# Kernel tuning notes

Measured on AMD Instinct MI355X. Metric: run time of the kernel, lower is better.

The kernel has to match this reference:

```python
import jax, jax.numpy as jnp
import numpy as np

B, T, D, H, E, O, A = 8192, 223, 7, 128, 50, 29, 9
IMPUTE_W, LABEL_W = 0.3, 1.0

def setup_inputs() -> dict:
    key = jax.random.key(0)
    ks = jax.random.split(key, 32)
    u = lambda k, shape, fan: jax.random.uniform(k, shape, jnp.float32, -1.0/np.sqrt(fan), 1.0/np.sqrt(fan))
    return {
        'values':    jax.random.normal(ks[0], (B, T, D), jnp.float32),
        'masks':     (jax.random.uniform(ks[1], (B, T, D)) < 0.8).astype(jnp.float32),
        'deltas':    jax.random.uniform(ks[2], (B, T, D), jnp.float32) * 5.0,
        'probs':     jax.nn.softmax(jax.random.normal(ks[3], (B, O), jnp.float32), axis=1),
        'ancillary': jax.random.normal(ks[4], (B, A), jnp.float32),
        'labels':    jax.random.randint(ks[5], (B,), 0, O, jnp.int32),
        'W_td_h': u(ks[6], (H, D), H),  'b_td_h': u(ks[7], (H,), H),
        'W_td_x': u(ks[8], (D, D), D),  'b_td_x': u(ks[9], (D,), D),
        'W_hist': u(ks[10], (D, H), H), 'b_hist': u(ks[11], (D,), H),
        'W_feat': u(ks[12], (D, D), D), 'b_feat': u(ks[13], (D,), D),
        'W_comb': u(ks[14], (D, 2*D), 2*D), 'b_comb': u(ks[15], (D,), 2*D),
        'W_ih': u(ks[16], (4*H, 2*D), H), 'W_hh': u(ks[17], (4*H, H), H),
        'b_ih': u(ks[18], (4*H,), H),     'b_hh': u(ks[19], (4*H,), H),
        'W_anc': u(ks[20], (E, A), A),    'b_anc': u(ks[21], (E,), A),
        'W_cat': u(ks[22], (H, H + E), H + E), 'b_cat': u(ks[23], (H,), H + E),
        'W_out': u(ks[24], (O, H), H),    'b_out': u(ks[25], (O,), H),
    }

def _rits_forward(values, masks, deltas, probs, ancillary,
                  W_td_h, b_td_h, W_td_x, b_td_x, W_hist, b_hist,
                  W_feat, b_feat, W_comb, b_comb, W_ih, W_hh, b_ih, b_hh,
                  W_anc, b_anc, W_cat, b_cat, W_out, b_out):
    Bn = values.shape[0]
    td_x_diag = jnp.diag(W_td_x)                     # diag=True decay uses only diagonal
    Wf = W_feat * (1.0 - jnp.eye(D, dtype=W_feat.dtype))

    def step(carry, xt):
        h, c, xl = carry
        x, m, d = xt                                  # each [B, D]
        gamma_h = jnp.exp(-jax.nn.relu(d @ W_td_h.T + b_td_h))   # [B, H]
        gamma_x = jnp.exp(-jax.nn.relu(d * td_x_diag + b_td_x))  # [B, D]
        h = h * gamma_h
        x_h = h @ W_hist.T + b_hist
        msum = jnp.sum(m) + 1e-5
        xl = xl + jnp.sum(jnp.abs(x - x_h) * m) / msum
        x_c = m * x + (1.0 - m) * x_h
        z_h = x_c @ Wf.T + b_feat
        xl = xl + jnp.sum(jnp.abs(x - z_h) * m) / msum
        alpha = jnp.concatenate([gamma_x, m], axis=1) @ W_comb.T + b_comb
        c_h = alpha * z_h + (1.0 - alpha) * x_h
        xl = xl + jnp.sum(jnp.abs(x - c_h) * m) / msum
        c_c = m * x + (1.0 - m) * c_h
        inputs = jnp.concatenate([c_c, m], axis=1)    # [B, 2D]
        gates = inputs @ W_ih.T + b_ih + h @ W_hh.T + b_hh  # [B, 4H]
        i, f, g, o = jnp.split(gates, 4, axis=1)
        c = jax.nn.sigmoid(f) * c + jax.nn.sigmoid(i) * jnp.tanh(g)
        h = jax.nn.sigmoid(o) * jnp.tanh(c)
        return (h, c, xl), c_c

    h0 = jnp.zeros((Bn, H), values.dtype)
    c0 = jnp.zeros((Bn, H), values.dtype)
    xs = (jnp.swapaxes(values, 0, 1), jnp.swapaxes(masks, 0, 1), jnp.swapaxes(deltas, 0, 1))
    (h, c, x_loss), imps = jax.lax.scan(step, (h0, c0, jnp.float32(0.0)), xs)
    imputations = jnp.swapaxes(imps, 0, 1)           # [B, T, D]

    x_loss = x_loss * IMPUTE_W
    anc = jax.nn.relu(ancillary @ W_anc.T + b_anc)
    h = jax.nn.relu(jnp.concatenate([h, anc], axis=1) @ W_cat.T + b_cat)
    y_h = jax.nn.softmax(h @ W_out.T + b_out, axis=1)
    y_loss = jnp.sum((y_h - probs) ** 2) / (Bn + 1e-5) * LABEL_W
    return x_loss, y_loss, x_loss + y_loss, y_h, imputations

def reference(values, masks, deltas, probs, ancillary, labels,
              W_td_h, b_td_h, W_td_x, b_td_x, W_hist, b_hist,
              W_feat, b_feat, W_comb, b_comb, W_ih, W_hh, b_ih, b_hh,
              W_anc, b_anc, W_cat, b_cat, W_out, b_out):
    x_loss, y_loss, loss, y_h, imputations = _rits_forward(
        values, masks, deltas, probs, ancillary,
        W_td_h, b_td_h, W_td_x, b_td_x, W_hist, b_hist,
        W_feat, b_feat, W_comb, b_comb, W_ih, W_hh, b_ih, b_hh,
        W_anc, b_anc, W_cat, b_cat, W_out, b_out)
    return (x_loss, y_loss, loss, y_h, imputations, labels)
```

## Files before the change

kernel.cpp:

```cpp
#include <hip/hip_runtime.h>
#include <math.h>

#define B_ 8192
#define T_ 223
#define D_ 7
#define H_ 128
#define E_ 50
#define O_ 29
#define A_ 9
#define TD_ (T_*D_)
#define NB 32
#define NTHR 512
#define MB 8
#define MS_BG 128

#define WS_MINV  0
#define WS_ACC   (WS_MINV + T_)
#define WS_WCATT (WS_ACC + 2)
#define WS_HFIN  (WS_WCATT + 178*H_)

#define OUT_YH  3
#define OUT_IMP (OUT_YH + B_*O_)
#define OUT_LAB (OUT_IMP + B_*T_*D_)

typedef __attribute__((ext_vector_type(8))) short short8;
typedef __attribute__((ext_vector_type(4))) float floatx4;
#define MFMA16(Av,Bv,Cv) __builtin_amdgcn_mfma_f32_16x16x32_bf16((Av),(Bv),(Cv),0,0,0)

__device__ __forceinline__ unsigned short f2bf(float f) {
    unsigned int u = __builtin_bit_cast(unsigned int, f);
    return (unsigned short)((u + 0x7FFFu + ((u >> 16) & 1u)) >> 16);
}
__device__ __forceinline__ float bf2f(unsigned short s) {
    unsigned int u = ((unsigned int)s) << 16;
    return __builtin_bit_cast(float, u);
}
__device__ __forceinline__ float rcp_(float x)  { return __builtin_amdgcn_rcpf(x); }
__device__ __forceinline__ float sigm(float x)  { return rcp_(1.f + __expf(-x)); }
__device__ __forceinline__ float tanh_(float x) { return 1.f - 2.f*rcp_(1.f + __expf(2.f*x)); }

__global__ void rits_prep(const float* __restrict__ W_cat, float* __restrict__ ws)
{
    int idx = blockIdx.x * 256 + threadIdx.x;
    if (idx < H_*178) {
        int j = idx / 178, k = idx - j*178;
        ws[WS_WCATT + k*H_ + j] = W_cat[idx];
    }
    if (idx < T_) ws[WS_MINV + idx] = 0.f;
    if (idx < 2) ws[WS_ACC + idx] = 0.f;
}

__global__ void rits_msum(const float* __restrict__ masks, float* __restrict__ ws)
{
    const int tc = blockIdx.x % 7;
    const int bg = blockIdx.x / 7;
    const int t0 = tc * 32;
    const int nt = (t0 + 32 <= T_) ? 32 : (T_ - t0);
    const int ncol = nt * D_;
    const int tid = threadIdx.x;
    __shared__ float sums[224];
    float s = 0.f;
    if (tid < ncol) {
        const int bpg = B_ / MS_BG;
        const float* p = masks + (size_t)bg * bpg * TD_ + (size_t)t0 * D_ + tid;
        #pragma unroll 4
        for (int b = 0; b < bpg; ++b) s += p[(size_t)b * TD_];
    }
    if (tid < 224) sums[tid] = (tid < ncol) ? s : 0.f;
    __syncthreads();
    if (tid < 32) {
        float r = 0.f;
        #pragma unroll
        for (int q = 0; q < 7; ++q) r += sums[tid*7 + q];
        if (t0 + tid < T_) atomicAdd(&ws[WS_MINV + t0 + tid], r);
    }
}

__global__ __launch_bounds__(NTHR, 2) void rits_main(
    const float* __restrict__ values, const float* __restrict__ masks, const float* __restrict__ deltas,
    const float* __restrict__ W_td_h, const float* __restrict__ b_td_h,
    const float* __restrict__ W_td_x, const float* __restrict__ b_td_x,
    const float* __restrict__ W_hist, const float* __restrict__ b_hist,
    const float* __restrict__ W_feat, const float* __restrict__ b_feat,
    const float* __restrict__ W_comb, const float* __restrict__ b_comb,
    const float* __restrict__ W_ih, const float* __restrict__ W_hh,
    const float* __restrict__ b_ih, const float* __restrict__ b_hh,
    float* __restrict__ ws, float* __restrict__ out)
{
    __shared__ __attribute__((aligned(16))) unsigned short hbuf[NB*168];
    __shared__ __attribute__((aligned(16))) unsigned short dbuf[NB*72];
    __shared__ __attribute__((aligned(16))) unsigned short whis_lds[16*136];
    __shared__ float xs[NB*8], msh[NB*8], dsl[NB*8];
    __shared__ float xh_l[NB*8], xc_l[NB*8], gx_l[NB*8];
    __shared__ float bhist_l[8], tdx_l[8], btdx_l[8];
    __shared__ float impbuf[NB*16*7];
    __shared__ float red[8];

    const int tid  = threadIdx.x;
    const int b0   = blockIdx.x * NB;
    const int lane = tid & 63;
    const int w    = tid >> 6;
    const int quad = lane >> 4;
    const int l15  = lane & 15;

    for (int i = tid; i < NB*168; i += NTHR) hbuf[i] = 0;
    for (int i = tid; i < NB*72;  i += NTHR) dbuf[i] = 0;
    for (int i = tid; i < 16*136; i += NTHR) {
        int r = i / 136, c = i - r*136;
        whis_lds[i] = (r < 7 && c < 128) ? f2bf(W_hist[r*H_ + c]) : 0;
    }
    if (tid < 8) {
        bhist_l[tid] = (tid < 7) ? b_hist[tid] : 0.f;
        tdx_l[tid]   = (tid < 7) ? W_td_x[tid*D_ + tid] : 0.f;
        btdx_l[tid]  = (tid < 7) ? b_td_x[tid] : 0.f;
    }

    short8 whhf[4][4];
    short8 winf[4];
    short8 wtdf;
    float  biasg_r[4][4];
    float  btdh_r[4];
    {
        union UU { short8 v; unsigned short u[8]; } fr;
        #pragma unroll
        for (int c = 0; c < 4; ++c) {
            const int j = (c*8 + w)*16 + l15;
            #pragma unroll
            for (int s = 0; s < 4; ++s) {
                const float* p = W_hh + j*H_ + s*32 + quad*8;
                #pragma unroll
                for (int e = 0; e < 8; ++e) fr.u[e] = f2bf(p[e]);
                whhf[c][s] = fr.v;
            }
            #pragma unroll
            for (int e = 0; e < 8; ++e) {
                int k = quad*8 + e;
                fr.u[e] = (k < 14) ? f2bf(W_ih[j*14 + k]) : (unsigned short)0;
            }
            winf[c] = fr.v;
            #pragma unroll
            for (int r = 0; r < 4; ++r) {
                int jj = (c*8 + w)*16 + quad*4 + r;
                biasg_r[c][r] = b_ih[jj] + b_hh[jj];
            }
        }
        #pragma unroll
        for (int e = 0; e < 8; ++e) {
            int k = quad*8 + e;
            fr.u[e] = (k < 7) ? f2bf(W_td_h[(w*16 + l15)*D_ + k]) : (unsigned short)0;
        }
        wtdf = fr.v;
        #pragma unroll
        for (int r = 0; r < 4; ++r) btdh_r[r] = b_td_h[w*16 + quad*4 + r];
    }

    const bool ldr = (tid < NB*D_);
    const int  lb  = tid / D_, li = tid - (tid/D_)*D_;
    float wfr[7], wcr[14], bfr = 0.f, bcr = 0.f;
    if (ldr) {
        #pragma unroll
        for (int k = 0; k < 7; ++k)  wfr[k] = (k == li) ? 0.f : W_feat[li*D_ + k];
        #pragma unroll
        for (int k = 0; k < 14; ++k) wcr[k] = W_comb[li*14 + k];
        bfr = b_feat[li];  bcr = b_comb[li];
    }

    float c_st[2][4] = {{0,0,0,0},{0,0,0,0}};
    float lacc = 0.f;

    const long gbase = (long)(b0 + lb)*TD_ + li;
    float rx = 0.f, rm = 0.f, rd = 0.f;
    if (ldr) { rx = values[gbase]; rm = masks[gbase]; rd = deltas[gbase]; }

    const float* msums = ws + WS_MINV;

    for (int t = 0; t < T_; ++t) {
        if (ldr) { xs[lb*8+li] = rx; msh[lb*8+li] = rm; dsl[lb*8+li] = rd; }
        __syncthreads();
        if (ldr) {
            if (t + 1 < T_) {
                const long g = gbase + (long)(t+1)*D_;
                rx = values[g]; rm = masks[g]; rd = deltas[g];
            }
            dbuf[lb*72 + li] = f2bf(rd);
        }

        floatx4 acc[4][2];
        #pragma unroll
        for (int c = 0; c < 4; ++c)
            #pragma unroll
            for (int nt = 0; nt < 2; ++nt) {
                floatx4 a = { biasg_r[c][0], biasg_r[c][1], biasg_r[c][2], biasg_r[c][3] };
                acc[c][nt] = a;
            }
        floatx4 xh0 = {0,0,0,0}, xh1 = {0,0,0,0};
        #pragma unroll
        for (int s = 0; s < 4; ++s) {
            short8 hb0 = *(const short8*)&hbuf[l15*168       + s*32 + quad*8];
            short8 hb1 = *(const short8*)&hbuf[(16+l15)*168  + s*32 + quad*8];
            #pragma unroll
            for (int c = 0; c < 4; ++c) {
                acc[c][0] = MFMA16(whhf[c][s], hb0, acc[c][0]);
                acc[c][1] = MFMA16(whhf[c][s], hb1, acc[c][1]);
            }
            if (w == 7) {
                short8 wh = *(const short8*)&whis_lds[l15*136 + s*32 + quad*8];
                xh0 = MFMA16(wh, hb0, xh0);
                xh1 = MFMA16(wh, hb1, xh1);
            }
        }
        if (w == 7 && quad < 2) {
            #pragma unroll
            for (int nt = 0; nt < 2; ++nt) {
                const int b = nt*16 + l15;
                floatx4 xv = nt ? xh1 : xh0;
                #pragma unroll
                for (int r = 0; r < 4; ++r) {
                    const int i = quad*4 + r;
                    if (i < 7) {
                        float xhv = xv[r] + bhist_l[i];
                        float x = xs[b*8+i], m = msh[b*8+i], d = dsl[b*8+i];
                        xh_l[b*8+i] = xhv;
                        xc_l[b*8+i] = m*x + (1.f-m)*xhv;
                        gx_l[b*8+i] = __expf(-fmaxf(fmaf(d, tdx_l[i], btdx_l[i]), 0.f));
                    }
                }
            }
        }
        __syncthreads();

        floatx4 g0 = {0,0,0,0}, g1 = {0,0,0,0};
        const bool dec = (t + 1 < T_);
        if (dec) {
            short8 df0 = *(const short8*)&dbuf[l15*72      + quad*8];
            short8 df1 = *(const short8*)&dbuf[(16+l15)*72 + quad*8];
            floatx4 z = {0,0,0,0};
            g0 = MFMA16(wtdf, df0, z);
            g1 = MFMA16(wtdf, df1, z);
        }

        if (ldr) {
            const int b = lb, i = li;
            const float invt = rcp_(msums[t] + 1e-5f);
            const float x = xs[b*8+i], m = msh[b*8+i];
            float zh = bfr;
            #pragma unroll
            for (int k = 0; k < 7; ++k) zh = fmaf(wfr[k], xc_l[b*8+k], zh);
            float al = bcr;
            #pragma unroll
            for (int k = 0; k < 7; ++k) al = fmaf(wcr[k],   gx_l[b*8+k], al);
            #pragma unroll
            for (int k = 0; k < 7; ++k) al = fmaf(wcr[7+k], msh[b*8+k], al);
            const float xhv = xh_l[b*8+i];
            const float ch  = al*zh + (1.f-al)*xhv;
            const float cc  = m*x + (1.f-m)*ch;
            impbuf[(b*16 + (t & 15))*7 + i] = cc;
            hbuf[b*168 + 128 + i] = f2bf(cc);
            hbuf[b*168 + 135 + i] = f2bf(m);
            lacc = fmaf((fabsf(x-xhv) + fabsf(x-zh) + fabsf(x-ch)) * m, invt, lacc);
        }
        __syncthreads();

        {
            short8 ib0 = *(const short8*)&hbuf[l15*168      + 128 + quad*8];
            short8 ib1 = *(const short8*)&hbuf[(16+l15)*168 + 128 + quad*8];
            #pragma unroll
            for (int c = 0; c < 4; ++c) {
                acc[c][0] = MFMA16(winf[c], ib0, acc[c][0]);
                acc[c][1] = MFMA16(winf[c], ib1, acc[c][1]);
            }
        }
        #pragma unroll
        for (int nt = 0; nt < 2; ++nt) {
            const int b = nt*16 + l15;
            floatx4 gg = nt ? g1 : g0;
            float hnv[4];
            #pragma unroll
            for (int r = 0; r < 4; ++r) {
                float ig = acc[0][nt][r], fg = acc[1][nt][r];
                float gv = acc[2][nt][r], og = acc[3][nt][r];
                float cn = sigm(fg)*c_st[nt][r] + sigm(ig)*tanh_(gv);
                c_st[nt][r] = cn;
                float hn = sigm(og)*tanh_(cn);
                if (dec) hn *= __expf(-fmaxf(gg[r] + btdh_r[r], 0.f));
                hnv[r] = hn;
            }
            uint2 pk;
            pk.x = (unsigned)f2bf(hnv[0]) | ((unsigned)f2bf(hnv[1]) << 16);
            pk.y = (unsigned)f2bf(hnv[2]) | ((unsigned)f2bf(hnv[3]) << 16);
            *(uint2*)&hbuf[b*168 + w*16 + quad*4] = pk;
        }

        if ((t & 15) == 15 || t == T_ - 1) {
            const int t0 = t & ~15;
            const int b  = tid >> 4, c16 = tid & 15;
            if (t0 + c16 <= t) {
                float* gp = out + (size_t)OUT_IMP + (size_t)(b0+b)*TD_ + (size_t)(t0+c16)*D_;
                const float* lp = &impbuf[(b*16 + c16)*7];
                #pragma unroll
                for (int e = 0; e < 7; ++e) gp[e] = lp[e];
            }
        }
    }
    __syncthreads();

    for (int off = 32; off > 0; off >>= 1) lacc += __shfl_down(lacc, off, 64);
    if ((tid & 63) == 0) red[tid >> 6] = lacc;
    __syncthreads();
    if (tid == 0) {
        float s = 0.f;
        #pragma unroll
        for (int q = 0; q < 8; ++q) s += red[q];
        atomicAdd(&ws[WS_ACC], s);
    }
    for (int i = tid; i < NB*H_; i += NTHR) {
        int b = i >> 7, j = i & 127;
        ws[WS_HFIN + (size_t)(b0+b)*H_ + j] = bf2f(hbuf[b*168 + j]);
    }
}

__global__ __launch_bounds__(128) void rits_head(
    const float* __restrict__ probs, const float* __restrict__ ancillary, const int* __restrict__ labels,
    const float* __restrict__ W_anc, const float* __restrict__ b_anc,
    const float* __restrict__ b_cat,
    const float* __restrict__ W_out, const float* __restrict__ b_out,
    float* __restrict__ ws, float* __restrict__ out)
{
    __shared__ float hb[MB*H_];
    __shared__ float ancl[MB*52];
    __shared__ float hc[MB*H_];
    __shared__ float lg[MB*32];
    __shared__ float smx[MB], sinv[MB], ysum[MB];
    __shared__ float sq[MB*32];
    const int tid = threadIdx.x;
    const int bb0 = blockIdx.x * MB;

    for (int i = tid; i < MB*H_; i += 128) hb[i] = ws[WS_HFIN + (size_t)bb0*H_ + i];
    for (int i = tid; i < MB*E_; i += 128) {
        int b = i / E_, e = i - b*E_;
        float s = b_anc[e];
        #pragma unroll
        for (int a = 0; a < A_; ++a) s = fmaf(ancillary[(bb0+b)*A_ + a], W_anc[e*A_ + a], s);
        ancl[b*52+e] = fmaxf(s, 0.f);
    }
    __syncthreads();
    {
        const int j = tid;
        float s[MB];
        #pragma unroll
        for (int b = 0; b < MB; ++b) s[b] = b_cat[j];
        const float* wc = ws + WS_WCATT;
        for (int k = 0; k < H_; ++k) {
            float wv = wc[k*H_ + j];
            #pragma unroll
            for (int b = 0; b < MB; ++b) s[b] = fmaf(hb[b*H_+k], wv, s[b]);
        }
        for (int k = 0; k < E_; ++k) {
            float wv = wc[(H_+k)*H_ + j];
            #pragma unroll
            for (int b = 0; b < MB; ++b) s[b] = fmaf(ancl[b*52+k], wv, s[b]);
        }
        #pragma unroll
        for (int b = 0; b < MB; ++b) hc[b*H_+j] = fmaxf(s[b], 0.f);
    }
    __syncthreads();
    for (int i = tid; i < MB*O_; i += 128) {
        int b = i / O_, o = i - b*O_;
        float s = b_out[o];
        for (int k = 0; k < H_; ++k) s = fmaf(hc[b*H_+k], W_out[o*H_+k], s);
        lg[b*32+o] = s;
    }
    __syncthreads();
    if (tid < MB) {
        float mx = -1e30f;
        for (int o = 0; o < O_; ++o) mx = fmaxf(mx, lg[tid*32+o]);
        float se = 0.f;
        for (int o = 0; o < O_; ++o) se += __expf(lg[tid*32+o] - mx);
        smx[tid] = mx; sinv[tid] = 1.f / se;
    }
    __syncthreads();
    for (int i = tid; i < MB*O_; i += 128) {
        int b = i / O_, o = i - b*O_;
        float y = __expf(lg[b*32+o] - smx[b]) * sinv[b];
        out[OUT_YH + (size_t)(bb0+b)*O_ + o] = y;
        float d = y - probs[(size_t)(bb0+b)*O_ + o];
        sq[b*32+o] = d*d;
    }
    __syncthreads();
    if (tid < MB) {
        float s = 0.f;
        for (int o = 0; o < O_; ++o) s += sq[tid*32+o];
        ysum[tid] = s;
        out[OUT_LAB + bb0 + tid] = (float)labels[bb0 + tid];
    }
    __syncthreads();
    if (tid == 0) {
        float s = 0.f;
        #pragma unroll
        for (int b = 0; b < MB; ++b) s += ysum[b];
        atomicAdd(&ws[WS_ACC+1], s);
    }
}

__global__ void rits_fin(const float* __restrict__ ws, float* __restrict__ out)
{
    if (blockIdx.x == 0 && threadIdx.x == 0) {
        float xl = ws[WS_ACC] * 0.3f;
        float yl = ws[WS_ACC+1] * (1.0f / (8192.0f + 1e-5f));
        out[0] = xl; out[1] = yl; out[2] = xl + yl;
    }
}

extern "C" void kernel_launch(void* const* d_in, const int* in_sizes, int n_in,
                              void* d_out, int out_size, void* d_ws, size_t ws_size,
                              hipStream_t stream)
{
    const float* values = (const float*)d_in[0];
    const float* masks  = (const float*)d_in[1];
    const float* deltas = (const float*)d_in[2];
    const float* probs  = (const float*)d_in[3];
    const float* ancil  = (const float*)d_in[4];
    const int*   labels = (const int*)  d_in[5];
    const float* W_td_h = (const float*)d_in[6];
    const float* b_td_h = (const float*)d_in[7];
    const float* W_td_x = (const float*)d_in[8];
    const float* b_td_x = (const float*)d_in[9];
    const float* W_hist = (const float*)d_in[10];
    const float* b_hist = (const float*)d_in[11];
    const float* W_feat = (const float*)d_in[12];
    const float* b_feat = (const float*)d_in[13];
    const float* W_comb = (const float*)d_in[14];
    const float* b_comb = (const float*)d_in[15];
    const float* W_ih   = (const float*)d_in[16];
    const float* W_hh   = (const float*)d_in[17];
    const float* b_ih   = (const float*)d_in[18];
    const float* b_hh   = (const float*)d_in[19];
    const float* W_anc  = (const float*)d_in[20];
    const float* b_anc  = (const float*)d_in[21];
    const float* W_cat  = (const float*)d_in[22];
    const float* b_cat  = (const float*)d_in[23];
    const float* W_out  = (const float*)d_in[24];
    const float* b_out  = (const float*)d_in[25];
    float* ws  = (float*)d_ws;
    float* out = (float*)d_out;

    hipLaunchKernelGGL(rits_prep, dim3((H_*178 + 255)/256), dim3(256), 0, stream, W_cat, ws);
    hipLaunchKernelGGL(rits_msum, dim3(7*MS_BG), dim3(256), 0, stream, masks, ws);
    hipLaunchKernelGGL(rits_main, dim3(B_/NB), dim3(NTHR), 0, stream,
                       values, masks, deltas, W_td_h, b_td_h, W_td_x, b_td_x,
                       W_hist, b_hist, W_feat, b_feat, W_comb, b_comb,
                       W_ih, W_hh, b_ih, b_hh, ws, out);
    hipLaunchKernelGGL(rits_head, dim3(B_/MB), dim3(128), 0, stream,
                       probs, ancil, labels, W_anc, b_anc, b_cat, W_out, b_out, ws, out);
    hipLaunchKernelGGL(rits_fin, dim3(1), dim3(1), 0, stream, ws, out);
}
```

Measured before the change: 933.8 us.

## Fold gate biases and mask input into MFMA, redistribute decay and xc compute

Folds the LSTM gate bias and the mask half of the input projection into one MFMA that runs earlier, using a buffer that holds mask, delta and a constant-one column. The temporal-decay bias moves into the decay MFMA the same way. The x_c and gamma_x work moves from the single wave-7 serial section to the per-element loader threads. Biases are now rounded to bf16 inside the MFMA, which costs some precision, and the critical section between barriers gets shorter.

```diff
diff --git a/kernel.cpp b/kernel.cpp
--- a/kernel.cpp
+++ b/kernel.cpp
@@ -88,11 +88,11 @@
     float* __restrict__ ws, float* __restrict__ out)
 {
     __shared__ __attribute__((aligned(16))) unsigned short hbuf[NB*168];
-    __shared__ __attribute__((aligned(16))) unsigned short dbuf[NB*72];
+    __shared__ __attribute__((aligned(16))) unsigned short bbuf[NB*32];
     __shared__ __attribute__((aligned(16))) unsigned short whis_lds[16*136];
-    __shared__ float xs[NB*8], msh[NB*8], dsl[NB*8];
-    __shared__ float xh_l[NB*8], xc_l[NB*8], gx_l[NB*8];
-    __shared__ float bhist_l[8], tdx_l[8], btdx_l[8];
+    __shared__ float xm_l[NB*18];
+    __shared__ float gx_l[NB*9];
+    __shared__ float xh_l[NB*10];
     __shared__ float impbuf[NB*16*7];
     __shared__ float red[8];
 
@@ -104,22 +104,22 @@
     const int l15  = lane & 15;
 
     for (int i = tid; i < NB*168; i += NTHR) hbuf[i] = 0;
-    for (int i = tid; i < NB*72;  i += NTHR) dbuf[i] = 0;
+    for (int i = tid; i < NB*32;  i += NTHR) bbuf[i] = 0;
     for (int i = tid; i < 16*136; i += NTHR) {
         int r = i / 136, c = i - r*136;
         whis_lds[i] = (r < 7 && c < 128) ? f2bf(W_hist[r*H_ + c]) : 0;
     }
-    if (tid < 8) {
-        bhist_l[tid] = (tid < 7) ? b_hist[tid] : 0.f;
-        tdx_l[tid]   = (tid < 7) ? W_td_x[tid*D_ + tid] : 0.f;
-        btdx_l[tid]  = (tid < 7) ? b_td_x[tid] : 0.f;
+    __syncthreads();
+    if (tid < NB) {
+        bbuf[tid*32 + 7]  = 0x3F80;
+        bbuf[tid*32 + 15] = 0x3F80;
     }
 
     short8 whhf[4][4];
-    short8 winf[4];
+    short8 winf_c[4];
+    short8 winf_mb[4];
     short8 wtdf;
-    float  biasg_r[4][4];
-    float  btdh_r[4];
+    float  bh_r[4];
     {
         union UU { short8 v; unsigned short u[8]; } fr;
         #pragma unroll
@@ -135,34 +135,44 @@
             #pragma unroll
             for (int e = 0; e < 8; ++e) {
                 int k = quad*8 + e;
-                fr.u[e] = (k < 14) ? f2bf(W_ih[j*14 + k]) : (unsigned short)0;
-            }
-            winf[c] = fr.v;
-            #pragma unroll
-            for (int r = 0; r < 4; ++r) {
-                int jj = (c*8 + w)*16 + quad*4 + r;
-                biasg_r[c][r] = b_ih[jj] + b_hh[jj];
-            }
-        }
+                fr.u[e] = (k < 7) ? f2bf(W_ih[j*14 + k]) : (unsigned short)0;
+            }
+            winf_c[c] = fr.v;
+            #pragma unroll
+            for (int e = 0; e < 8; ++e) {
+                int k = quad*8 + e;
+                float v = (k < 7) ? W_ih[j*14 + 7 + k]
+                        : ((k == 7) ? (b_ih[j] + b_hh[j]) : 0.f);
+                fr.u[e] = f2bf(v);
+            }
+            winf_mb[c] = fr.v;
+        }
+        const int j2 = w*16 + l15;
         #pragma unroll
         for (int e = 0; e < 8; ++e) {
             int k = quad*8 + e;
-            fr.u[e] = (k < 7) ? f2bf(W_td_h[(w*16 + l15)*D_ + k]) : (unsigned short)0;
+            float v = (k >= 8 && k < 15) ? W_td_h[j2*D_ + (k - 8)]
+                    : ((k == 15) ? b_td_h[j2] : 0.f);
+            fr.u[e] = f2bf(v);
         }
         wtdf = fr.v;
         #pragma unroll
-        for (int r = 0; r < 4; ++r) btdh_r[r] = b_td_h[w*16 + quad*4 + r];
+        for (int r = 0; r < 4; ++r) {
+            int f = quad*4 + r;
+            bh_r[r] = (quad < 2 && f < 7) ? b_hist[f] : 0.f;
+        }
     }
 
     const bool ldr = (tid < NB*D_);
     const int  lb  = tid / D_, li = tid - (tid/D_)*D_;
-    float wfr[7], wcr[14], bfr = 0.f, bcr = 0.f;
+    float wfr[7], wcr[14], bfr = 0.f, bcr = 0.f, tdx_own = 0.f, btdx_own = 0.f;
     if (ldr) {
         #pragma unroll
         for (int k = 0; k < 7; ++k)  wfr[k] = (k == li) ? 0.f : W_feat[li*D_ + k];
         #pragma unroll
         for (int k = 0; k < 14; ++k) wcr[k] = W_comb[li*14 + k];
         bfr = b_feat[li];  bcr = b_comb[li];
+        tdx_own = W_td_x[li*D_ + li];  btdx_own = b_td_x[li];
     }
 
     float c_st[2][4] = {{0,0,0,0},{0,0,0,0}};
@@ -175,24 +185,24 @@
     const float* msums = ws + WS_MINV;
 
     for (int t = 0; t < T_; ++t) {
-        if (ldr) { xs[lb*8+li] = rx; msh[lb*8+li] = rm; dsl[lb*8+li] = rd; }
+        if (ldr) {
+            float2 s2 = { rx, rm };
+            *(float2*)&xm_l[lb*18 + 2*li] = s2;
+            gx_l[lb*9 + li] = __expf(-fmaxf(fmaf(rd, tdx_own, btdx_own), 0.f));
+            bbuf[lb*32 + li] = f2bf(rm);
+        }
         __syncthreads();
-        if (ldr) {
-            if (t + 1 < T_) {
-                const long g = gbase + (long)(t+1)*D_;
-                rx = values[g]; rm = masks[g]; rd = deltas[g];
-            }
-            dbuf[lb*72 + li] = f2bf(rd);
+        if (ldr && t + 1 < T_) {
+            const long g = gbase + (long)(t+1)*D_;
+            rx = values[g]; rm = masks[g]; rd = deltas[g];
+            bbuf[lb*32 + 8 + li] = f2bf(rd);
         }
 
         floatx4 acc[4][2];
         #pragma unroll
         for (int c = 0; c < 4; ++c)
             #pragma unroll
-            for (int nt = 0; nt < 2; ++nt) {
-                floatx4 a = { biasg_r[c][0], biasg_r[c][1], biasg_r[c][2], biasg_r[c][3] };
-                acc[c][nt] = a;
-            }
+            for (int nt = 0; nt < 2; ++nt) { floatx4 z = {0,0,0,0}; acc[c][nt] = z; }
         floatx4 xh0 = {0,0,0,0}, xh1 = {0,0,0,0};
         #pragma unroll
         for (int s = 0; s < 4; ++s) {
@@ -214,49 +224,51 @@
             for (int nt = 0; nt < 2; ++nt) {
                 const int b = nt*16 + l15;
                 floatx4 xv = nt ? xh1 : xh0;
-                #pragma unroll
-                for (int r = 0; r < 4; ++r) {
-                    const int i = quad*4 + r;
-                    if (i < 7) {
-                        float xhv = xv[r] + bhist_l[i];
-                        float x = xs[b*8+i], m = msh[b*8+i], d = dsl[b*8+i];
-                        xh_l[b*8+i] = xhv;
-                        xc_l[b*8+i] = m*x + (1.f-m)*xhv;
-                        gx_l[b*8+i] = __expf(-fmaxf(fmaf(d, tdx_l[i], btdx_l[i]), 0.f));
-                    }
-                }
+                float2 p0 = { xv[0] + bh_r[0], xv[1] + bh_r[1] };
+                float2 p1 = { xv[2] + bh_r[2], xv[3] + bh_r[3] };
+                *(float2*)&xh_l[b*10 + quad*4]     = p0;
+                *(float2*)&xh_l[b*10 + quad*4 + 2] = p1;
             }
         }
         __syncthreads();
 
+        const bool dec = (t + 1 < T_);
         floatx4 g0 = {0,0,0,0}, g1 = {0,0,0,0};
-        const bool dec = (t + 1 < T_);
-        if (dec) {
-            short8 df0 = *(const short8*)&dbuf[l15*72      + quad*8];
-            short8 df1 = *(const short8*)&dbuf[(16+l15)*72 + quad*8];
-            floatx4 z = {0,0,0,0};
-            g0 = MFMA16(wtdf, df0, z);
-            g1 = MFMA16(wtdf, df1, z);
+        {
+            short8 bb0 = *(const short8*)&bbuf[l15*32      + quad*8];
+            short8 bb1 = *(const short8*)&bbuf[(16+l15)*32 + quad*8];
+            #pragma unroll
+            for (int c = 0; c < 4; ++c) {
+                acc[c][0] = MFMA16(winf_mb[c], bb0, acc[c][0]);
+                acc[c][1] = MFMA16(winf_mb[c], bb1, acc[c][1]);
+            }
+            if (dec) {
+                floatx4 z = {0,0,0,0};
+                g0 = MFMA16(wtdf, bb0, z);
+                g1 = MFMA16(wtdf, bb1, z);
+            }
         }
 
         if (ldr) {
             const int b = lb, i = li;
             const float invt = rcp_(msums[t] + 1e-5f);
-            const float x = xs[b*8+i], m = msh[b*8+i];
-            float zh = bfr;
-            #pragma unroll
-            for (int k = 0; k < 7; ++k) zh = fmaf(wfr[k], xc_l[b*8+k], zh);
-            float al = bcr;
-            #pragma unroll
-            for (int k = 0; k < 7; ++k) al = fmaf(wcr[k],   gx_l[b*8+k], al);
-            #pragma unroll
-            for (int k = 0; k < 7; ++k) al = fmaf(wcr[7+k], msh[b*8+k], al);
-            const float xhv = xh_l[b*8+i];
-            const float ch  = al*zh + (1.f-al)*xhv;
-            const float cc  = m*x + (1.f-m)*ch;
+            const float x = xm_l[b*18 + 2*i], m = xm_l[b*18 + 2*i + 1];
+            const float xhv = xh_l[b*10 + i];
+            float zh = bfr, al = bcr;
+            #pragma unroll
+            for (int k = 0; k < 7; ++k) {
+                const float xk  = xm_l[b*18 + 2*k];
+                const float mk  = xm_l[b*18 + 2*k + 1];
+                const float xhk = xh_l[b*10 + k];
+                const float xck = mk*xk + (1.f - mk)*xhk;
+                zh = fmaf(wfr[k], xck, zh);
+                al = fmaf(wcr[k], gx_l[b*9 + k], al);
+                al = fmaf(wcr[7+k], mk, al);
+            }
+            const float ch = al*zh + (1.f - al)*xhv;
+            const float cc = m*x + (1.f - m)*ch;
             impbuf[(b*16 + (t & 15))*7 + i] = cc;
             hbuf[b*168 + 128 + i] = f2bf(cc);
-            hbuf[b*168 + 135 + i] = f2bf(m);
             lacc = fmaf((fabsf(x-xhv) + fabsf(x-zh) + fabsf(x-ch)) * m, invt, lacc);
         }
         __syncthreads();
@@ -266,8 +278,8 @@
             short8 ib1 = *(const short8*)&hbuf[(16+l15)*168 + 128 + quad*8];
             #pragma unroll
             for (int c = 0; c < 4; ++c) {
-                acc[c][0] = MFMA16(winf[c], ib0, acc[c][0]);
-                acc[c][1] = MFMA16(winf[c], ib1, acc[c][1]);
+                acc[c][0] = MFMA16(winf_c[c], ib0, acc[c][0]);
+                acc[c][1] = MFMA16(winf_c[c], ib1, acc[c][1]);
             }
         }
         #pragma unroll
@@ -282,7 +294,7 @@
                 float cn = sigm(fg)*c_st[nt][r] + sigm(ig)*tanh_(gv);
                 c_st[nt][r] = cn;
                 float hn = sigm(og)*tanh_(cn);
-                if (dec) hn *= __expf(-fmaxf(gg[r] + btdh_r[r], 0.f));
+                if (dec) hn *= __expf(-fmaxf(gg[r], 0.f));
                 hnv[r] = hn;
             }
             uint2 pk;
```

New measurement: 925.6 us. Within noise of the previous version (-0.9%).
